# Performance work log

Measured on AMD Instinct MI355X. Metric: run time of the kernel, lower is better.

The kernel has to match this reference:

```python
import jax, jax.numpy as jnp
import numpy as np

N = 100000    # nodes
DEG = 16      # in-degree per node
E = N * DEG   # edges
F = 128       # in_channels == hidden_channels


def setup_inputs() -> dict:
    key = jax.random.key(0)
    ks = jax.random.split(key, 8)
    x = jax.random.normal(ks[0], (N, F), dtype=jnp.float32)
    src = jax.random.randint(ks[1], (E,), 0, N, dtype=jnp.int32)
    dst = jnp.repeat(jnp.arange(N, dtype=jnp.int32), DEG)  # every dst has in-degree DEG
    edge_index = jnp.stack([src, dst])  # [2, E]
    s = 0.05
    W0 = jax.random.normal(ks[2], (F, F), dtype=jnp.float32) * s
    b0 = jax.random.normal(ks[3], (F,), dtype=jnp.float32) * s
    Wr0 = jax.random.normal(ks[4], (F, F), dtype=jnp.float32) * s
    W1 = jax.random.normal(ks[5], (F, F), dtype=jnp.float32) * s
    b1 = jax.random.normal(ks[6], (F,), dtype=jnp.float32) * s
    Wr1 = jax.random.normal(ks[7], (F, F), dtype=jnp.float32) * s
    return {"x": x, "edge_index": edge_index, "W0": W0, "b0": b0, "Wr0": Wr0,
            "W1": W1, "b1": b1, "Wr1": Wr1}


def reference(x, edge_index, W0, b0, Wr0, W1, b1, Wr1):
    src, dst = edge_index[0], edge_index[1]
    n = x.shape[0]
    # in-degree per destination node == matmul(adj_t, ones) (constant across feature dim)
    deg = jax.ops.segment_sum(jnp.ones((src.shape[0],), x.dtype), dst, num_segments=n)

    def layer(h, W, b, Wr):
        # SpMM: agg[j] = sum over edges (i->j) of h[i]   (binary adjacency, aggr='add')
        agg = jax.ops.segment_sum(h[src], dst, num_segments=n)  # [N, F]
        out = agg @ W.T + b + h @ Wr.T   # lin(agg) + lin_r(x_target)
        out = jax.nn.relu(out)           # activation=True; dropout=0 (eval)
        # adj_norm_: out -= matmul(adj_t, h) / matmul(adj_t, ones) = agg / deg
        return out - agg / deg[:, None]

    x = layer(x, W0, b0, Wr0)
    x = layer(x, W1, b1, Wr1)
    return x
```

## Files before the change

### kernel.cpp

```cpp
#include <hip/hip_runtime.h>


#define N_NODES 100000
#define DEG 16
#define F 128
#define K2 256
#define TILE 32
#define LDP 264

typedef __attribute__((ext_vector_type(8))) short short8;
typedef __attribute__((ext_vector_type(4))) float f32x4;
typedef __attribute__((ext_vector_type(4))) unsigned short us4;
typedef __attribute__((ext_vector_type(8))) unsigned short us8;

__device__ __forceinline__ unsigned short f2bf(float f) {
    unsigned u = __builtin_bit_cast(unsigned, f);
    u += 0x7FFFu + ((u >> 16) & 1u);
    return (unsigned short)(u >> 16);
}
__device__ __forceinline__ float bf2f(unsigned short h) {
    return __builtin_bit_cast(float, (unsigned)h << 16);
}

__global__ void cast_x_kernel(const float* __restrict__ x, unsigned short* __restrict__ xb) {
    int i = blockIdx.x * blockDim.x + threadIdx.x;
    const float4 v = ((const float4*)x)[i];
    us4 o; o.x = f2bf(v.x); o.y = f2bf(v.y); o.z = f2bf(v.z); o.w = f2bf(v.w);
    ((us4*)xb)[i] = o;
}

__global__ void build_bt_kernel(const float* __restrict__ W0, const float* __restrict__ Wr0,
                                const float* __restrict__ W1, const float* __restrict__ Wr1,
                                unsigned short* __restrict__ Bt) {
    int t = blockIdx.x * 256 + threadIdx.x;
    int layer = t >> 15;
    int n = (t >> 8) & 127;
    int k = t & 255;
    const float* W  = layer ? W1  : W0;
    const float* Wr = layer ? Wr1 : Wr0;
    float v = (k < 128) ? W[n * 128 + k] : Wr[n * 128 + (k - 128)];
    Bt[t] = f2bf(v);
}

__global__ __launch_bounds__(256, 8) void layer_kernel(
    const unsigned short* __restrict__ hb,
    const unsigned short* __restrict__ Bt,
    const float* __restrict__ bias,
    const int* __restrict__ src,
    unsigned short* __restrict__ outb,
    float* __restrict__ outf)
{
    __shared__ unsigned short sIn[TILE][LDP];
    const int tid = threadIdx.x;
    const int r0 = blockIdx.x * TILE;

    const int g16 = tid >> 4, l16 = tid & 15;
    const int wbase = tid & 48;
    #pragma unroll
    for (int i = 0; i < 2; ++i) {
        const int trow = g16 * 2 + i;
        const int grow = r0 + trow;
        const int su = src[grow * DEG + l16];
        float a0 = 0.f, a1 = 0.f, a2 = 0.f, a3 = 0.f,
              a4 = 0.f, a5 = 0.f, a6 = 0.f, a7 = 0.f;
        #pragma unroll
        for (int e = 0; e < DEG; ++e) {
            int idx = __shfl(su, wbase + e);
            us8 hv = *(const us8*)(hb + (size_t)idx * F + l16 * 8);
            a0 += bf2f(hv[0]); a1 += bf2f(hv[1]); a2 += bf2f(hv[2]); a3 += bf2f(hv[3]);
            a4 += bf2f(hv[4]); a5 += bf2f(hv[5]); a6 += bf2f(hv[6]); a7 += bf2f(hv[7]);
        }
        us8 o;
        o[0] = f2bf(a0); o[1] = f2bf(a1); o[2] = f2bf(a2); o[3] = f2bf(a3);
        o[4] = f2bf(a4); o[5] = f2bf(a5); o[6] = f2bf(a6); o[7] = f2bf(a7);
        *(us8*)&sIn[trow][l16 * 8] = o;
        *(us8*)&sIn[trow][128 + l16 * 8] = *(const us8*)(hb + (size_t)grow * F + l16 * 8);
    }
    __syncthreads();

    const int w = tid >> 6, wl = tid & 63;
    const int lc = wl & 15;
    const int kb = (wl >> 4) * 8;
    const int rt = w >> 1;
    const int cfb = (w & 1) * 4;
    f32x4 acc[4];
    #pragma unroll
    for (int cf = 0; cf < 4; ++cf) acc[cf] = (f32x4){0.f, 0.f, 0.f, 0.f};

    #pragma unroll
    for (int ks = 0; ks < 8; ++ks) {
        short8 af = *(const short8*)&sIn[rt * 16 + lc][ks * 32 + kb];
        #pragma unroll
        for (int cf = 0; cf < 4; ++cf) {
            short8 bfr = *(const short8*)(Bt + (size_t)((cfb + cf) * 16 + lc) * K2 + ks * 32 + kb);
            acc[cf] = __builtin_amdgcn_mfma_f32_16x16x32_bf16(af, bfr, acc[cf], 0, 0, 0);
        }
    }

    const int rbase = (wl >> 4) * 4;
    #pragma unroll
    for (int cf = 0; cf < 4; ++cf) {
        const int col = (cfb + cf) * 16 + lc;
        const float bv = bias[col];
        #pragma unroll
        for (int j = 0; j < 4; ++j) {
            const int trow = rt * 16 + rbase + j;
            const int grow = r0 + trow;
            float v = fmaxf(acc[cf][j] + bv, 0.f) - bf2f(sIn[trow][col]) * (1.0f / DEG);
            if (outb) outb[(size_t)grow * F + col] = f2bf(v);
            else      outf[(size_t)grow * F + col] = v;
        }
    }
}

extern "C" void kernel_launch(void* const* d_in, const int* in_sizes, int n_in,
                              void* d_out, int out_size, void* d_ws, size_t ws_size,
                              hipStream_t stream) {
    const float* x   = (const float*)d_in[0];
    const int*   ei  = (const int*)d_in[1];
    const float* W0  = (const float*)d_in[2];
    const float* b0  = (const float*)d_in[3];
    const float* Wr0 = (const float*)d_in[4];
    const float* W1  = (const float*)d_in[5];
    const float* b1  = (const float*)d_in[6];
    const float* Wr1 = (const float*)d_in[7];
    const int* src = ei;

    unsigned short* xb  = (unsigned short*)d_ws;
    unsigned short* h1b = xb  + (size_t)N_NODES * F;
    unsigned short* Bt  = h1b + (size_t)N_NODES * F;

    cast_x_kernel<<<(N_NODES * F / 4 + 255) / 256, 256, 0, stream>>>(x, xb);
    build_bt_kernel<<<256, 256, 0, stream>>>(W0, Wr0, W1, Wr1, Bt);

    const int nb = N_NODES / TILE;
    layer_kernel<<<nb, 256, 0, stream>>>(xb,  Bt,         b0, src, h1b,    nullptr);
    layer_kernel<<<nb, 256, 0, stream>>>(h1b, Bt + 32768, b1, src, nullptr, (float*)d_out);
}
```

Before: 181.7 us.

## Slice features per XCD so gather tables fit L2; split aggregation from matmul

Node features are now stored as 8 slices of 16 bf16 features each, 32 bytes per node per slice. A new aggregation kernel sends slice blockIdx&7 to each block, so with round-robin block dispatch each XCD gathers from one 3.2MB slice that can stay resident in its L2. The gather uses inline-asm loads with a 6-deep software pipeline and waitcnt control. Aggregation and the matmul epilogue are now separate kernels, and the cast and weight-prep kernels are merged into one. The cost is an extra write and read of the aggregated features through memory, and the L2 benefit relies on the hardware's block-to-XCD mapping.

```diff
diff --git a/kernel.cpp b/kernel.cpp
--- a/kernel.cpp
+++ b/kernel.cpp
@@ -5,13 +5,15 @@
 #define DEG 16
 #define F 128
 #define K2 256
-#define TILE 32
+#define SLF 16
 #define LDP 264
 
 typedef __attribute__((ext_vector_type(8))) short short8;
 typedef __attribute__((ext_vector_type(4))) float f32x4;
 typedef __attribute__((ext_vector_type(4))) unsigned short us4;
 typedef __attribute__((ext_vector_type(8))) unsigned short us8;
+typedef __attribute__((ext_vector_type(4))) unsigned int uint4v;
+typedef __attribute__((ext_vector_type(4))) int int4v;
 
 __device__ __forceinline__ unsigned short f2bf(float f) {
     unsigned u = __builtin_bit_cast(unsigned, f);
@@ -21,60 +23,141 @@
 __device__ __forceinline__ float bf2f(unsigned short h) {
     return __builtin_bit_cast(float, (unsigned)h << 16);
 }
-
-__global__ void cast_x_kernel(const float* __restrict__ x, unsigned short* __restrict__ xb) {
-    int i = blockIdx.x * blockDim.x + threadIdx.x;
-    const float4 v = ((const float4*)x)[i];
-    us4 o; o.x = f2bf(v.x); o.y = f2bf(v.y); o.z = f2bf(v.z); o.w = f2bf(v.w);
-    ((us4*)xb)[i] = o;
-}
-
-__global__ void build_bt_kernel(const float* __restrict__ W0, const float* __restrict__ Wr0,
-                                const float* __restrict__ W1, const float* __restrict__ Wr1,
-                                unsigned short* __restrict__ Bt) {
-    int t = blockIdx.x * 256 + threadIdx.x;
-    int layer = t >> 15;
-    int n = (t >> 8) & 127;
-    int k = t & 255;
-    const float* W  = layer ? W1  : W0;
-    const float* Wr = layer ? Wr1 : Wr0;
-    float v = (k < 128) ? W[n * 128 + k] : Wr[n * 128 + (k - 128)];
-    Bt[t] = f2bf(v);
-}
-
-__global__ __launch_bounds__(256, 8) void layer_kernel(
-    const unsigned short* __restrict__ hb,
+__device__ __forceinline__ float bflo(unsigned u) {
+    return __builtin_bit_cast(float, u << 16);
+}
+__device__ __forceinline__ float bfhi(unsigned u) {
+    return __builtin_bit_cast(float, u & 0xffff0000u);
+}
+
+#define GLOADT(dst, off) \
+    asm volatile("global_load_dwordx4 %0, %1, %2" \
+                 : "=v"(dst) : "v"(off), "s"(tab) : "memory")
+
+#define VMWAIT(n) do { \
+    asm volatile("s_waitcnt vmcnt(" #n ")" ::: "memory"); \
+    __builtin_amdgcn_sched_barrier(0); } while (0)
+
+#define CONSUME(q) do { \
+    a0 += bflo((q)[0]); a1 += bfhi((q)[0]); \
+    a2 += bflo((q)[1]); a3 += bfhi((q)[1]); \
+    a4 += bflo((q)[2]); a5 += bfhi((q)[2]); \
+    a6 += bflo((q)[3]); a7 += bfhi((q)[3]); } while (0)
+
+__global__ void prep_kernel(const float* __restrict__ x, unsigned short* __restrict__ xs,
+                            const float* __restrict__ W0, const float* __restrict__ Wr0,
+                            const float* __restrict__ W1, const float* __restrict__ Wr1,
+                            unsigned short* __restrict__ Bt) {
+    if (blockIdx.x < 256) {
+        int t = blockIdx.x * 256 + threadIdx.x;
+        int layer = t >> 15;
+        int n = (t >> 8) & 127;
+        int k = t & 255;
+        const float* W  = layer ? W1  : W0;
+        const float* Wr = layer ? Wr1 : Wr0;
+        float v = (k < 128) ? W[n * 128 + k] : Wr[n * 128 + (k - 128)];
+        Bt[t] = f2bf(v);
+    } else {
+        const int b = (int)blockIdx.x - 256;
+        const int node = b * 64 + ((int)threadIdx.x >> 2);
+        if (node < N_NODES) {
+            const int q = threadIdx.x & 3;
+            const float4* xp = (const float4*)(x + (size_t)node * F + q * 32);
+            float4 v[8];
+            #pragma unroll
+            for (int j = 0; j < 8; ++j) v[j] = xp[j];
+            us8 a0, a1, b0, b1;
+            #pragma unroll
+            for (int j = 0; j < 2; ++j) {
+                const float4 p0 = v[j * 2], p1 = v[j * 2 + 1];
+                const float4 p2 = v[4 + j * 2], p3 = v[4 + j * 2 + 1];
+                us8* lo = j ? &a1 : &a0;
+                us8* hi = j ? &b1 : &b0;
+                (*lo)[0]=f2bf(p0.x); (*lo)[1]=f2bf(p0.y); (*lo)[2]=f2bf(p0.z); (*lo)[3]=f2bf(p0.w);
+                (*lo)[4]=f2bf(p1.x); (*lo)[5]=f2bf(p1.y); (*lo)[6]=f2bf(p1.z); (*lo)[7]=f2bf(p1.w);
+                (*hi)[0]=f2bf(p2.x); (*hi)[1]=f2bf(p2.y); (*hi)[2]=f2bf(p2.z); (*hi)[3]=f2bf(p2.w);
+                (*hi)[4]=f2bf(p3.x); (*hi)[5]=f2bf(p3.y); (*hi)[6]=f2bf(p3.z); (*hi)[7]=f2bf(p3.w);
+            }
+            const size_t oA = ((size_t)(2 * q) * N_NODES + node) * SLF;
+            const size_t oB = ((size_t)(2 * q + 1) * N_NODES + node) * SLF;
+            *(us8*)(xs + oA)     = a0;
+            *(us8*)(xs + oA + 8) = a1;
+            *(us8*)(xs + oB)     = b0;
+            *(us8*)(xs + oB + 8) = b1;
+        }
+    }
+}
+
+__global__ __launch_bounds__(256, 7) void agg_kernel(
+    const unsigned short* __restrict__ hs,
+    const int* __restrict__ src,
+    unsigned short* __restrict__ aggs)
+{
+    const int s = blockIdx.x & 7;
+    const int chunk = blockIdx.x >> 3;
+    const int t = threadIdx.x;
+    const int r = chunk * 128 + (t >> 1);
+    if (r >= N_NODES) return;
+    const unsigned pb = (unsigned)(t & 1) * 16u;
+    const unsigned short* tab = hs + (size_t)s * ((size_t)N_NODES * SLF);
+
+    const int4v* sp = (const int4v*)(src + (size_t)r * DEG);
+    const int4v i0 = __builtin_nontemporal_load(sp);
+    const int4v i1 = __builtin_nontemporal_load(sp + 1);
+    const int4v i2 = __builtin_nontemporal_load(sp + 2);
+    const int4v i3 = __builtin_nontemporal_load(sp + 3);
+    unsigned vo[16];
+    vo[0]  = (unsigned)i0[0] * 32u + pb;  vo[1]  = (unsigned)i0[1] * 32u + pb;
+    vo[2]  = (unsigned)i0[2] * 32u + pb;  vo[3]  = (unsigned)i0[3] * 32u + pb;
+    vo[4]  = (unsigned)i1[0] * 32u + pb;  vo[5]  = (unsigned)i1[1] * 32u + pb;
+    vo[6]  = (unsigned)i1[2] * 32u + pb;  vo[7]  = (unsigned)i1[3] * 32u + pb;
+    vo[8]  = (unsigned)i2[0] * 32u + pb;  vo[9]  = (unsigned)i2[1] * 32u + pb;
+    vo[10] = (unsigned)i2[2] * 32u + pb;  vo[11] = (unsigned)i2[3] * 32u + pb;
+    vo[12] = (unsigned)i3[0] * 32u + pb;  vo[13] = (unsigned)i3[1] * 32u + pb;
+    vo[14] = (unsigned)i3[2] * 32u + pb;  vo[15] = (unsigned)i3[3] * 32u + pb;
+    __builtin_amdgcn_sched_barrier(0);
+
+    float a0 = 0.f, a1 = 0.f, a2 = 0.f, a3 = 0.f,
+          a4 = 0.f, a5 = 0.f, a6 = 0.f, a7 = 0.f;
+    uint4v q[6];
+    #pragma unroll
+    for (int e = 0; e < 6; ++e) GLOADT(q[e], vo[e]);
+    #pragma unroll
+    for (int e = 0; e < 10; ++e) {
+        VMWAIT(5); CONSUME(q[e % 6]); GLOADT(q[e % 6], vo[e + 6]);
+    }
+    VMWAIT(5); CONSUME(q[4]);
+    VMWAIT(4); CONSUME(q[5]);
+    VMWAIT(3); CONSUME(q[0]);
+    VMWAIT(2); CONSUME(q[1]);
+    VMWAIT(1); CONSUME(q[2]);
+    VMWAIT(0); CONSUME(q[3]);
+
+    us8 o;
+    o[0] = f2bf(a0); o[1] = f2bf(a1); o[2] = f2bf(a2); o[3] = f2bf(a3);
+    o[4] = f2bf(a4); o[5] = f2bf(a5); o[6] = f2bf(a6); o[7] = f2bf(a7);
+    __builtin_nontemporal_store(o, (us8*)(aggs + ((size_t)s * N_NODES + r) * SLF + (pb >> 1)));
+}
+
+__global__ __launch_bounds__(256, 8) void mm_kernel(
+    const unsigned short* __restrict__ hs,
+    const unsigned short* __restrict__ aggs,
     const unsigned short* __restrict__ Bt,
     const float* __restrict__ bias,
-    const int* __restrict__ src,
-    unsigned short* __restrict__ outb,
+    unsigned short* __restrict__ outs,
     float* __restrict__ outf)
 {
-    __shared__ unsigned short sIn[TILE][LDP];
+    __shared__ unsigned short sIn[32][LDP];
     const int tid = threadIdx.x;
-    const int r0 = blockIdx.x * TILE;
-
-    const int g16 = tid >> 4, l16 = tid & 15;
-    const int wbase = tid & 48;
-    #pragma unroll
-    for (int i = 0; i < 2; ++i) {
-        const int trow = g16 * 2 + i;
-        const int grow = r0 + trow;
-        const int su = src[grow * DEG + l16];
-        float a0 = 0.f, a1 = 0.f, a2 = 0.f, a3 = 0.f,
-              a4 = 0.f, a5 = 0.f, a6 = 0.f, a7 = 0.f;
-        #pragma unroll
-        for (int e = 0; e < DEG; ++e) {
-            int idx = __shfl(su, wbase + e);
-            us8 hv = *(const us8*)(hb + (size_t)idx * F + l16 * 8);
-            a0 += bf2f(hv[0]); a1 += bf2f(hv[1]); a2 += bf2f(hv[2]); a3 += bf2f(hv[3]);
-            a4 += bf2f(hv[4]); a5 += bf2f(hv[5]); a6 += bf2f(hv[6]); a7 += bf2f(hv[7]);
-        }
-        us8 o;
-        o[0] = f2bf(a0); o[1] = f2bf(a1); o[2] = f2bf(a2); o[3] = f2bf(a3);
-        o[4] = f2bf(a4); o[5] = f2bf(a5); o[6] = f2bf(a6); o[7] = f2bf(a7);
-        *(us8*)&sIn[trow][l16 * 8] = o;
-        *(us8*)&sIn[trow][128 + l16 * 8] = *(const us8*)(hb + (size_t)grow * F + l16 * 8);
+    const int r0 = blockIdx.x * 32;
+
+    {
+        const int p = tid >> 5, rr = tid & 31;
+        const size_t o = ((size_t)p * N_NODES + (r0 + rr)) * SLF;
+        *(us8*)&sIn[rr][p * 16]           = *(const us8*)(aggs + o);
+        *(us8*)&sIn[rr][p * 16 + 8]       = *(const us8*)(aggs + o + 8);
+        *(us8*)&sIn[rr][128 + p * 16]     = *(const us8*)(hs + o);
+        *(us8*)&sIn[rr][128 + p * 16 + 8] = *(const us8*)(hs + o + 8);
     }
     __syncthreads();
 
@@ -105,10 +188,10 @@
         #pragma unroll
         for (int j = 0; j < 4; ++j) {
             const int trow = rt * 16 + rbase + j;
-            const int grow = r0 + trow;
+            const int gr = r0 + trow;
             float v = fmaxf(acc[cf][j] + bv, 0.f) - bf2f(sIn[trow][col]) * (1.0f / DEG);
-            if (outb) outb[(size_t)grow * F + col] = f2bf(v);
-            else      outf[(size_t)grow * F + col] = v;
+            if (outs) outs[((size_t)(col >> 4) * N_NODES + gr) * SLF + (col & 15)] = f2bf(v);
+            else      outf[(size_t)gr * F + col] = v;
         }
     }
 }
@@ -126,14 +209,17 @@
     const float* Wr1 = (const float*)d_in[7];
     const int* src = ei;
 
-    unsigned short* xb  = (unsigned short*)d_ws;
-    unsigned short* h1b = xb  + (size_t)N_NODES * F;
-    unsigned short* Bt  = h1b + (size_t)N_NODES * F;
-
-    cast_x_kernel<<<(N_NODES * F / 4 + 255) / 256, 256, 0, stream>>>(x, xb);
-    build_bt_kernel<<<256, 256, 0, stream>>>(W0, Wr0, W1, Wr1, Bt);
-
-    const int nb = N_NODES / TILE;
-    layer_kernel<<<nb, 256, 0, stream>>>(xb,  Bt,         b0, src, h1b,    nullptr);
-    layer_kernel<<<nb, 256, 0, stream>>>(h1b, Bt + 32768, b1, src, nullptr, (float*)d_out);
-}
+    unsigned short* xs   = (unsigned short*)d_ws;
+    unsigned short* aggs = xs + (size_t)N_NODES * F;
+    unsigned short* Bt   = aggs + (size_t)N_NODES * F;
+
+    prep_kernel<<<256 + (N_NODES + 63) / 64, 256, 0, stream>>>(x, xs, W0, Wr0, W1, Wr1, Bt);
+
+    const int nb1 = 8 * ((N_NODES + 127) / 128);
+    const int nb2 = N_NODES / 32;
+
+    agg_kernel<<<nb1, 256, 0, stream>>>(xs, src, aggs);
+    mm_kernel<<<nb2, 256, 0, stream>>>(xs, aggs, Bt, b0, xs, nullptr);
+    agg_kernel<<<nb1, 256, 0, stream>>>(xs, src, aggs);
+    mm_kernel<<<nb2, 256, 0, stream>>>(xs, aggs, Bt + 32768, b1, nullptr, (float*)d_out);
+}
```

Result: slower. 283.8 us (+56.2%).
